# Kernel optimization log

Measured on AMD Instinct MI355X. Metric: run time of the kernel, lower is better.

The kernel has to match this reference:

```python
import jax, jax.numpy as jnp
import numpy as np

N, E, EMB, EDGE, ITERS = 50000, 400000, 128, 32, 2
EPS = 1e-5


def setup_inputs() -> dict:
    key = jax.random.key(0)
    ks = jax.random.split(key, 8)
    s = 0.05

    def lin(k, i, o):
        return jax.random.normal(k, (i, o), jnp.float32) * s

    def mlp_params(k):
        k1, k2 = jax.random.split(k)
        return dict(W1=lin(k1, 2 * EMB + EDGE, EMB), b1=jnp.zeros((EMB,)),
                    g1=jnp.ones((EMB,)), be1=jnp.zeros((EMB,)),
                    W2=lin(k2, EMB, EMB), b2=jnp.zeros((EMB,)),
                    g2=jnp.ones((EMB,)), be2=jnp.zeros((EMB,)))

    p = mlp_params(ks[3])
    c = mlp_params(ks[4])
    inp = {
        'nodes': jax.random.normal(ks[0], (N, EMB), jnp.float32),
        'edges': jax.random.randint(ks[1], (2, E), 0, N, jnp.int64),
        'edge_attr': jax.random.normal(ks[2], (E, EDGE), jnp.float32),
        'fW': lin(ks[5], EMB, EMB), 'fb': jnp.zeros((EMB,)),
        'fg': jnp.ones((EMB,)), 'fbe': jnp.zeros((EMB,)),
    }
    for name, d in (('p', p), ('c', c)):
        for kk, v in d.items():
            inp[name + kk] = v
    return inp


def _bn(x, g, b):
    # training-mode BatchNorm1d: batch stats over axis 0, biased variance
    m = x.mean(0)
    v = x.var(0)
    return (x - m) * jax.lax.rsqrt(v + EPS) * g + b


def _edge_mlp(h, W1, b1, g1, be1, W2, b2, g2, be2):
    h = jax.nn.relu(_bn(h @ W1 + b1, g1, be1))
    return jax.nn.relu(_bn(h @ W2 + b2, g2, be2))


def _agg(x, idx_i, idx_j, ea, params):
    # message: mlp([x_i, x_j, edge_attr]); aggregate sum at idx_i; degree-normalize
    msg = _edge_mlp(jnp.concatenate([x[idx_i], x[idx_j], ea], axis=1), *params)
    summed = jax.ops.segment_sum(msg, idx_i, num_segments=x.shape[0])
    deg = jax.ops.segment_sum(jnp.ones(idx_i.shape, x.dtype), idx_i,
                              num_segments=x.shape[0])
    deg_inv = jnp.where(deg > 0, 1.0 / deg, 0.0)
    return summed * deg_inv[:, None]


def reference(nodes, edges, edge_attr,
              pW1, pb1, pg1, pbe1, pW2, pb2, pg2, pbe2,
              cW1, cb1, cg1, cbe1, cW2, cb2, cg2, cbe2,
              fW, fb, fg, fbe):
    src, dst = edges[0], edges[1]
    pp = (pW1, pb1, pg1, pbe1, pW2, pb2, pg2, pbe2)
    cp = (cW1, cb1, cg1, cbe1, cW2, cb2, cg2, cbe2)
    for _ in range(ITERS):
        fi = _agg(nodes, dst, src, edge_attr, pp)  # parent: source_to_target
        fo = _agg(nodes, src, dst, edge_attr, cp)  # child: target_to_source
        upd = jax.nn.relu(_bn((nodes + fi + fo) @ fW + fb, fg, fbe))
        nodes = nodes + upd
    return nodes
```

## Files before the change

### kernel.cpp

```cpp
#include <hip/hip_runtime.h>
#include <math.h>

#define NN 50000
#define EE 400000
#define EMBD 128
#define KIN 288
#define NITERS 2
#define EPSV 1e-5f
#define SAE 296
#define SA1 136
#define NT_E 6250
#define G0P 1024
#define G1 1024

typedef __attribute__((ext_vector_type(8))) short bf16x8;
typedef __attribute__((ext_vector_type(4))) float f32x4;

#define MFMA16(a, b, c) __builtin_amdgcn_mfma_f32_16x16x32_bf16(a, b, c, 0, 0, 0)

__device__ __forceinline__ unsigned short f2bf(float x) {
  unsigned int u = __float_as_uint(x);
  u += 0x7fffu + ((u >> 16) & 1u);
  return (unsigned short)(u >> 16);
}

__device__ __forceinline__ int physch(int ch, int row) {
  return (ch < 32) ? ((ch & ~7) | ((ch ^ (row & 7)) & 7)) : ch;
}


__global__ void k_zeroi(int* __restrict__ p, int n) {
  for (int i = blockIdx.x * blockDim.x + threadIdx.x; i < n;
       i += gridDim.x * blockDim.x)
    p[i] = 0;
}

__global__ void k_detect(const long long* __restrict__ e64, int* __restrict__ flag) {
  __shared__ int ok;
  if (threadIdx.x == 0) ok = 1;
  __syncthreads();
  for (int i = threadIdx.x; i < 4096; i += blockDim.x) {
    const long long v = e64[i];
    if (v < 0 || v >= NN) atomicAnd(&ok, 0);
  }
  __syncthreads();
  if (threadIdx.x == 0) *flag = ok;
}

__global__ void k_convert(const void* __restrict__ edges, const int* __restrict__ flag,
                          int* __restrict__ src, int* __restrict__ dst) {
  const int is64 = *flag;
  for (int i = blockIdx.x * blockDim.x + threadIdx.x; i < 2 * EE;
       i += gridDim.x * blockDim.x) {
    const int v = is64 ? (int)((const long long*)edges)[i] : ((const int*)edges)[i];
    if (i < EE) src[i] = v; else dst[i - EE] = v;
  }
}

__global__ void k_count(const int* __restrict__ src, const int* __restrict__ dst,
                        int* __restrict__ degp, int* __restrict__ degc) {
  for (int e = blockIdx.x * blockDim.x + threadIdx.x; e < EE;
       e += gridDim.x * blockDim.x) {
    atomicAdd(&degp[dst[e]], 1);
    atomicAdd(&degc[src[e]], 1);
  }
}

__global__ void k_dinv(const int* __restrict__ dp, const int* __restrict__ dc,
                       float* __restrict__ ip, float* __restrict__ ic) {
  for (int n = blockIdx.x * blockDim.x + threadIdx.x; n < NN;
       n += gridDim.x * blockDim.x) {
    ip[n] = dp[n] ? 1.f / (float)dp[n] : 0.f;
    ic[n] = dc[n] ? 1.f / (float)dc[n] : 0.f;
  }
}

__global__ __launch_bounds__(1024) void k_scan2(
    const int* __restrict__ degp, const int* __restrict__ degc,
    int* __restrict__ offp, int* __restrict__ offc) {
  const int* deg = blockIdx.x ? degc : degp;
  int* off = blockIdx.x ? offc : offp;
  __shared__ int sh[1024];
  const int t = threadIdx.x;
  const int i0 = t * 49;
  int s = 0;
#pragma unroll 1
  for (int k = 0; k < 49; ++k) {
    const int i = i0 + k;
    if (i < NN) s += deg[i];
  }
  sh[t] = s;
  __syncthreads();
  for (int o = 1; o < 1024; o <<= 1) {
    const int y = (t >= o) ? sh[t - o] : 0;
    __syncthreads();
    sh[t] += y;
    __syncthreads();
  }
  int base = sh[t] - s;
#pragma unroll 1
  for (int k = 0; k < 49; ++k) {
    const int i = i0 + k;
    if (i < NN) {
      off[i] = base;
      base += deg[i];
    }
  }
  if (t == 1023) off[NN] = sh[1023];
}

__global__ void k_copycur(const int* __restrict__ offp, const int* __restrict__ offc,
                          int* __restrict__ curp, int* __restrict__ curc) {
  for (int i = blockIdx.x * blockDim.x + threadIdx.x; i < NN;
       i += gridDim.x * blockDim.x) {
    curp[i] = offp[i];
    curc[i] = offc[i];
  }
}

__global__ void k_scatter(const int* __restrict__ src, const int* __restrict__ dst,
                          int* __restrict__ curp, int* __restrict__ curc,
                          int* __restrict__ lstp, int* __restrict__ lstc) {
  for (int e = blockIdx.x * blockDim.x + threadIdx.x; e < EE;
       e += gridDim.x * blockDim.x) {
    const int pp = atomicAdd(&curp[dst[e]], 1);
    lstp[pp] = e;
    const int pc = atomicAdd(&curc[src[e]], 1);
    lstc[pc] = e;
  }
}

__global__ void k_initnodes(const float* __restrict__ in, float* __restrict__ nd,
                            unsigned short* __restrict__ xb) {
  const int tot = NN * EMBD / 4;
  for (int i = blockIdx.x * blockDim.x + threadIdx.x; i < tot;
       i += gridDim.x * blockDim.x) {
    const float4 v = ((const float4*)in)[i];
    ((float4*)nd)[i] = v;
    short4 b;
    b.x = (short)f2bf(v.x); b.y = (short)f2bf(v.y);
    b.z = (short)f2bf(v.z); b.w = (short)f2bf(v.w);
    *(short4*)&xb[(size_t)i * 4] = b;
  }
}

__global__ void k_prepW(const float* __restrict__ W, unsigned short* __restrict__ Wt,
                        int K) {
  const int idx = blockIdx.x * blockDim.x + threadIdx.x;
  if (idx < K * EMBD) {
    const int k = idx >> 7, n = idx & 127;
    Wt[(size_t)n * K + k] = f2bf(W[(size_t)k * EMBD + n]);
  }
}

__global__ void k_prepea(const float* __restrict__ ea,
                         unsigned short* __restrict__ eab) {
  const int tot = EE * 32 / 8;
  for (int i = blockIdx.x * blockDim.x + threadIdx.x; i < tot;
       i += gridDim.x * blockDim.x) {
    const float4 a = ((const float4*)ea)[i * 2];
    const float4 b = ((const float4*)ea)[i * 2 + 1];
    union { unsigned short u[8]; uint4 v; } o;
    o.u[0] = f2bf(a.x); o.u[1] = f2bf(a.y); o.u[2] = f2bf(a.z); o.u[3] = f2bf(a.w);
    o.u[4] = f2bf(b.x); o.u[5] = f2bf(b.y); o.u[6] = f2bf(b.z); o.u[7] = f2bf(b.w);
    ((uint4*)eab)[i] = o.v;
  }
}


template <int EAB>
__global__ __launch_bounds__(256, 1) void k_pass0m(
    const unsigned short* __restrict__ xb,
    const int* __restrict__ i0, const int* __restrict__ j0,
    const unsigned short* __restrict__ W0, float* __restrict__ st0,
    unsigned short* __restrict__ Y0,
    const int* __restrict__ i1, const int* __restrict__ j1,
    const unsigned short* __restrict__ W1, float* __restrict__ st1,
    unsigned short* __restrict__ Y1,
    const float* __restrict__ ea, const unsigned short* __restrict__ eab,
    const int nb0) {
  __shared__ __align__(16) unsigned short Ab[64 * SAE];
  __shared__ float red[256];
  const int phase = (blockIdx.x >= nb0) ? 1 : 0;
  const int* __restrict__ idx_i = phase ? i1 : i0;
  const int* __restrict__ idx_j = phase ? j1 : j0;
  const unsigned short* __restrict__ W1t = phase ? W1 : W0;
  float* __restrict__ stat = phase ? st1 : st0;
  unsigned short* __restrict__ Y = phase ? Y1 : Y0;
  const int stride = phase ? ((int)gridDim.x - nb0) : nb0;
  const int t = threadIdx.x;
  const int lane = t & 63, w = t >> 6, m = lane & 15, kg = lane >> 4;
  const int r = t >> 2, sub = t & 3;
  const int n0 = w * 32 + m, n1 = n0 + 16;
  bf16x8 B0[9], B1[9];
#pragma unroll
  for (int ks = 0; ks < 9; ++ks) {
    B0[ks] = *(const bf16x8*)&W1t[(size_t)n0 * KIN + ks * 32 + kg * 8];
    B1[ks] = *(const bf16x8*)&W1t[(size_t)n1 * KIN + ks * 32 + kg * 8];
  }
  float s0 = 0.f, s1 = 0.f, q0 = 0.f, q1 = 0.f;
  int tile = blockIdx.x - phase * nb0;
  int inext = idx_i[tile * 64 + r];
  int jnext = idx_j[tile * 64 + r];
  while (tile < NT_E) {
    const int icur = inext, jcur = jnext;
    __syncthreads();
    {
      const uint4* xi = (const uint4*)(xb + (size_t)icur * EMBD);
      const uint4* xj = (const uint4*)(xb + (size_t)jcur * EMBD);
      unsigned short* rowp = &Ab[r * SAE];
#pragma unroll
      for (int qq = 0; qq < 8; ++qq) {
        const int c = sub + qq * 4;
        const uint4 v = (c < 16) ? xi[c] : xj[c - 16];
        *(uint4*)&rowp[physch(c, r) * 8] = v;
      }
      const int e = tile * 64 + r;
      uint4 ev;
      if (EAB) {
        ev = *(const uint4*)&eab[(size_t)e * 32 + sub * 8];
      } else {
        const float4 e0 = *(const float4*)&ea[(size_t)e * 32 + sub * 8];
        const float4 e1 = *(const float4*)&ea[(size_t)e * 32 + sub * 8 + 4];
        union { unsigned short u[8]; uint4 v4; } o;
        o.u[0] = f2bf(e0.x); o.u[1] = f2bf(e0.y); o.u[2] = f2bf(e0.z);
        o.u[3] = f2bf(e0.w); o.u[4] = f2bf(e1.x); o.u[5] = f2bf(e1.y);
        o.u[6] = f2bf(e1.z); o.u[7] = f2bf(e1.w);
        ev = o.v4;
      }
      *(uint4*)&rowp[(32 + sub) * 8] = ev;
    }
    __syncthreads();
    const int next = tile + stride;
    if (next < NT_E) {
      inext = idx_i[next * 64 + r];
      jnext = idx_j[next * 64 + r];
    }
    const f32x4 zz = {0.f, 0.f, 0.f, 0.f};
    f32x4 acc[4][2] = {{zz, zz}, {zz, zz}, {zz, zz}, {zz, zz}};
#pragma unroll
    for (int ks = 0; ks < 9; ++ks) {
      const int aoff = physch(ks * 4 + kg, m) * 8;
#pragma unroll
      for (int mt = 0; mt < 4; ++mt) {
        const bf16x8 a = *(const bf16x8*)&Ab[(mt * 16 + m) * SAE + aoff];
        acc[mt][0] = MFMA16(a, B0[ks], acc[mt][0]);
        acc[mt][1] = MFMA16(a, B1[ks], acc[mt][1]);
      }
    }
#pragma unroll
    for (int mt = 0; mt < 4; ++mt)
#pragma unroll
      for (int r2 = 0; r2 < 4; ++r2) {
        const float v0 = acc[mt][0][r2], v1 = acc[mt][1][r2];
        s0 += v0; q0 += v0 * v0;
        s1 += v1; q1 += v1 * v1;
      }
    __syncthreads();
#pragma unroll
    for (int nt = 0; nt < 2; ++nt) {
      const int c = w * 32 + nt * 16 + m;
      const int cc = c >> 3, cl = c & 7;
#pragma unroll
      for (int mt = 0; mt < 4; ++mt)
#pragma unroll
        for (int r2 = 0; r2 < 4; ++r2) {
          const int rw = mt * 16 + kg * 4 + r2;
          Ab[rw * SAE + physch(cc, rw) * 8 + cl] = f2bf(acc[mt][nt][r2]);
        }
    }
    __syncthreads();
    unsigned short* Yt = Y + (size_t)tile * 64 * EMBD;
#pragma unroll
    for (int i = 0; i < 4; ++i) {
      const int g = i * 2048 + t * 8;
      const int row = g >> 7, ch = (g >> 3) & 15;
      *(uint4*)&Yt[g] = *(const uint4*)&Ab[row * SAE + physch(ch, row) * 8];
    }
    tile = next;
  }
  s0 += __shfl_xor(s0, 16); s0 += __shfl_xor(s0, 32);
  q0 += __shfl_xor(q0, 16); q0 += __shfl_xor(q0, 32);
  s1 += __shfl_xor(s1, 16); s1 += __shfl_xor(s1, 32);
  q1 += __shfl_xor(q1, 16); q1 += __shfl_xor(q1, 32);
  if (kg == 0) {
    const int c0 = w * 32 + m, c1 = c0 + 16;
    red[c0] = s0; red[128 + c0] = q0;
    red[c1] = s1; red[128 + c1] = q1;
  }
  __syncthreads();
  if (t < 128) {
    atomicAdd(&stat[t], red[t]);
    atomicAdd(&stat[128 + t], red[128 + t]);
  }
}


__device__ __forceinline__ void pass1_body(
    const unsigned short* __restrict__ W2t, float* __restrict__ stat,
    unsigned short* __restrict__ Y, int tile, const int stride) {
  __shared__ __align__(16) unsigned short Ab[64 * SA1];
  __shared__ float red[256];
  const int t = threadIdx.x;
  const int lane = t & 63, w = t >> 6, m = lane & 15, kg = lane >> 4;
  const int n0 = w * 32 + m, n1 = n0 + 16;
  const int ch = t & 15;
  bf16x8 B0[4], B1[4];
#pragma unroll
  for (int ks = 0; ks < 4; ++ks) {
    B0[ks] = *(const bf16x8*)&W2t[(size_t)n0 * EMBD + ks * 32 + kg * 8];
    B1[ks] = *(const bf16x8*)&W2t[(size_t)n1 * EMBD + ks * 32 + kg * 8];
  }
  float scr[8], shr[8];
#pragma unroll
  for (int h = 0; h < 8; ++h) {
    scr[h] = stat[256 + ch * 8 + h];
    shr[h] = stat[384 + ch * 8 + h];
  }
  float s0 = 0.f, s1 = 0.f, q0 = 0.f, q1 = 0.f;
  uint4 yreg[4];
  {
    const unsigned short* Yt = Y + (size_t)tile * 64 * EMBD;
#pragma unroll
    for (int i = 0; i < 4; ++i)
      yreg[i] = *(const uint4*)&Yt[i * 2048 + t * 8];
  }
  while (tile < NT_E) {
    __syncthreads();
#pragma unroll
    for (int i = 0; i < 4; ++i) {
      const int row = i * 16 + (t >> 4);
      const unsigned int* pv = (const unsigned int*)&yreg[i];
      union { unsigned short u[8]; uint4 v; } o;
#pragma unroll
      for (int h = 0; h < 4; ++h) {
        const unsigned int pw = pv[h];
        const float f0 = __uint_as_float(pw << 16);
        const float f1 = __uint_as_float(pw & 0xffff0000u);
        o.u[h * 2] = f2bf(fmaxf(fmaf(f0, scr[h * 2], shr[h * 2]), 0.f));
        o.u[h * 2 + 1] = f2bf(fmaxf(fmaf(f1, scr[h * 2 + 1], shr[h * 2 + 1]), 0.f));
      }
      *(uint4*)&Ab[row * SA1 + physch(ch, row) * 8] = o.v;
    }
    __syncthreads();
    const int next = tile + stride;
    if (next < NT_E) {
      const unsigned short* Yt = Y + (size_t)next * 64 * EMBD;
#pragma unroll
      for (int i = 0; i < 4; ++i)
        yreg[i] = *(const uint4*)&Yt[i * 2048 + t * 8];
    }
    const f32x4 zz = {0.f, 0.f, 0.f, 0.f};
    f32x4 acc[4][2] = {{zz, zz}, {zz, zz}, {zz, zz}, {zz, zz}};
#pragma unroll
    for (int ks = 0; ks < 4; ++ks) {
      const int aoff = physch(ks * 4 + kg, m) * 8;
#pragma unroll
      for (int mt = 0; mt < 4; ++mt) {
        const bf16x8 a = *(const bf16x8*)&Ab[(mt * 16 + m) * SA1 + aoff];
        acc[mt][0] = MFMA16(a, B0[ks], acc[mt][0]);
        acc[mt][1] = MFMA16(a, B1[ks], acc[mt][1]);
      }
    }
#pragma unroll
    for (int mt = 0; mt < 4; ++mt)
#pragma unroll
      for (int r2 = 0; r2 < 4; ++r2) {
        const float v0 = acc[mt][0][r2], v1 = acc[mt][1][r2];
        s0 += v0; q0 += v0 * v0;
        s1 += v1; q1 += v1 * v1;
      }
    __syncthreads();
#pragma unroll
    for (int nt = 0; nt < 2; ++nt) {
      const int c = w * 32 + nt * 16 + m;
      const int cc = c >> 3, cl = c & 7;
#pragma unroll
      for (int mt = 0; mt < 4; ++mt)
#pragma unroll
        for (int r2 = 0; r2 < 4; ++r2) {
          const int rw = mt * 16 + kg * 4 + r2;
          Ab[rw * SA1 + physch(cc, rw) * 8 + cl] = f2bf(acc[mt][nt][r2]);
        }
    }
    __syncthreads();
    unsigned short* Yo = Y + (size_t)tile * 64 * EMBD;
#pragma unroll
    for (int i = 0; i < 4; ++i) {
      const int g = i * 2048 + t * 8;
      const int row = g >> 7, c2 = (g >> 3) & 15;
      *(uint4*)&Yo[g] = *(const uint4*)&Ab[row * SA1 + physch(c2, row) * 8];
    }
    tile = next;
  }
  s0 += __shfl_xor(s0, 16); s0 += __shfl_xor(s0, 32);
  q0 += __shfl_xor(q0, 16); q0 += __shfl_xor(q0, 32);
  s1 += __shfl_xor(s1, 16); s1 += __shfl_xor(s1, 32);
  q1 += __shfl_xor(q1, 16); q1 += __shfl_xor(q1, 32);
  if (kg == 0) {
    const int c0 = w * 32 + m, c1 = c0 + 16;
    red[c0] = s0; red[128 + c0] = q0;
    red[c1] = s1; red[128 + c1] = q1;
  }
  __syncthreads();
  if (t < 128) {
    atomicAdd(&stat[512 + t], red[t]);
    atomicAdd(&stat[640 + t], red[128 + t]);
  }
}

__global__ __launch_bounds__(256, 3) void k_pass1(
    const unsigned short* __restrict__ W2t, float* __restrict__ stat,
    unsigned short* __restrict__ Y) {
  pass1_body(W2t, stat, Y, blockIdx.x, G1);
}

__global__ __launch_bounds__(256, 3) void k_pass1m(
    const unsigned short* __restrict__ Wp, const unsigned short* __restrict__ Wc,
    float* __restrict__ statP, float* __restrict__ statC,
    unsigned short* __restrict__ Yp, unsigned short* __restrict__ Yc) {
  const int phase = (blockIdx.x >= G1) ? 1 : 0;
  const unsigned short* W2t = phase ? Wc : Wp;
  float* stat = phase ? statC : statP;
  unsigned short* Y = phase ? Yc : Yp;
  pass1_body(W2t, stat, Y, blockIdx.x - phase * G1, G1);
}


__global__ __launch_bounds__(256) void k_aggm(
    const unsigned short* __restrict__ Yp, const unsigned short* __restrict__ Yc,
    const int* __restrict__ offp, const int* __restrict__ lstp,
    const int* __restrict__ offc, const int* __restrict__ lstc,
    const float* __restrict__ statP, const float* __restrict__ statC,
    const float* __restrict__ dinvp, const float* __restrict__ dinvc,
    float* __restrict__ agg) {
  const int n = blockIdx.x * 4 + (threadIdx.x >> 6);
  const int lane = threadIdx.x & 63;
  if (n >= NN) return;
  float r0, r1;
  {
    const int o0 = offp[n], o1 = offp[n + 1];
    const float sc0 = statP[768 + 2 * lane], sc1 = statP[768 + 2 * lane + 1];
    const float sh0 = statP[896 + 2 * lane], sh1 = statP[896 + 2 * lane + 1];
    float a0 = 0.f, a1 = 0.f;
    for (int o = o0; o < o1; ++o) {
      const int e = lstp[o];
      const unsigned int pw = ((const unsigned int*)(Yp + (size_t)e * EMBD))[lane];
      a0 += fmaxf(fmaf(__uint_as_float(pw << 16), sc0, sh0), 0.f);
      a1 += fmaxf(fmaf(__uint_as_float(pw & 0xffff0000u), sc1, sh1), 0.f);
    }
    const float d = dinvp[n];
    r0 = a0 * d;
    r1 = a1 * d;
  }
  {
    const int o0 = offc[n], o1 = offc[n + 1];
    const float sc0 = statC[768 + 2 * lane], sc1 = statC[768 + 2 * lane + 1];
    const float sh0 = statC[896 + 2 * lane], sh1 = statC[896 + 2 * lane + 1];
    float a0 = 0.f, a1 = 0.f;
    for (int o = o0; o < o1; ++o) {
      const int e = lstc[o];
      const unsigned int pw = ((const unsigned int*)(Yc + (size_t)e * EMBD))[lane];
      a0 += fmaxf(fmaf(__uint_as_float(pw << 16), sc0, sh0), 0.f);
      a1 += fmaxf(fmaf(__uint_as_float(pw & 0xffff0000u), sc1, sh1), 0.f);
    }
    const float d = dinvc[n];
    r0 += a0 * d;
    r1 += a1 * d;
  }
  float2 out;
  out.x = r0;
  out.y = r1;
  ((float2*)(agg + (size_t)n * EMBD))[lane] = out;
}

template <int ADD>
__global__ __launch_bounds__(256) void k_agg2(
    const unsigned short* __restrict__ Y2, const int* __restrict__ off,
    const int* __restrict__ lst, const float* __restrict__ stat,
    const float* __restrict__ dinv, float* __restrict__ agg) {
  const int n = blockIdx.x * 4 + (threadIdx.x >> 6);
  const int lane = threadIdx.x & 63;
  if (n >= NN) return;
  const int o0 = off[n], o1 = off[n + 1];
  const float sc0 = stat[768 + 2 * lane], sc1 = stat[768 + 2 * lane + 1];
  const float sh0 = stat[896 + 2 * lane], sh1 = stat[896 + 2 * lane + 1];
  float a0 = 0.f, a1 = 0.f;
  for (int o = o0; o < o1; ++o) {
    const int e = lst[o];
    const unsigned int pw = ((const unsigned int*)(Y2 + (size_t)e * EMBD))[lane];
    a0 += fmaxf(fmaf(__uint_as_float(pw << 16), sc0, sh0), 0.f);
    a1 += fmaxf(fmaf(__uint_as_float(pw & 0xffff0000u), sc1, sh1), 0.f);
  }
  const float d = dinv[n];
  float2 out;
  if (ADD) {
    const float2 prev = ((const float2*)(agg + (size_t)n * EMBD))[lane];
    out.x = prev.x + a0 * d;
    out.y = prev.y + a1 * d;
  } else {
    out.x = a0 * d;
    out.y = a1 * d;
  }
  ((float2*)(agg + (size_t)n * EMBD))[lane] = out;
}


template <int NK, bool SWZ>
__device__ __forceinline__ void gemm_g(const unsigned short* Ab, const int sa,
                                       const unsigned short* __restrict__ Wt,
                                       const int K, const int m, const int kg,
                                       const int w, f32x4 acc[4][2]) {
  const int n0 = w * 32 + m, n1 = n0 + 16;
#pragma unroll
  for (int ks = 0; ks < NK; ++ks) {
    const int koff = ks * 32 + kg * 8;
    const int aoff = SWZ ? physch(koff >> 3, m) * 8 : koff;
    const bf16x8 b0 = *(const bf16x8*)&Wt[(size_t)n0 * K + koff];
    const bf16x8 b1 = *(const bf16x8*)&Wt[(size_t)n1 * K + koff];
#pragma unroll
    for (int mt = 0; mt < 4; ++mt) {
      const bf16x8 a = *(const bf16x8*)&Ab[(mt * 16 + m) * sa + aoff];
      acc[mt][0] = MFMA16(a, b0, acc[mt][0]);
      acc[mt][1] = MFMA16(a, b1, acc[mt][1]);
    }
  }
}

__device__ __forceinline__ void stats_epi64(const f32x4 acc[4][2], float* red,
                                            float* __restrict__ statg, const int t,
                                            const int m, const int kg, const int w) {
#pragma unroll
  for (int nt = 0; nt < 2; ++nt) {
    float s = 0.f, q = 0.f;
#pragma unroll
    for (int mt = 0; mt < 4; ++mt)
#pragma unroll
      for (int r = 0; r < 4; ++r) {
        const float v = acc[mt][nt][r];
        s += v;
        q += v * v;
      }
    s += __shfl_xor(s, 16); s += __shfl_xor(s, 32);
    q += __shfl_xor(q, 16); q += __shfl_xor(q, 32);
    if (kg == 0) {
      const int c = w * 32 + nt * 16 + m;
      red[c] = s;
      red[128 + c] = q;
    }
  }
  __syncthreads();
  if (t < 128) {
    atomicAdd(&statg[t], red[t]);
    atomicAdd(&statg[128 + t], red[128 + t]);
  }
}

__global__ __launch_bounds__(256) void k_node(
    const float* __restrict__ nd, float* __restrict__ ag,
    const unsigned short* __restrict__ Wt, float* __restrict__ stat) {
  __shared__ __align__(16) unsigned short Ab[64 * SA1];
  __shared__ float red[256];
  const int t = threadIdx.x;
  const int n0 = blockIdx.x * 64;
  {
    const int r = t >> 2, sub = t & 3;
    const int row = n0 + r;
    unsigned short* drow = &Ab[r * SA1];
#pragma unroll
    for (int q = 0; q < 8; ++q) {
      const int c4 = sub + q * 4;
      float4 va;
      if (row < NN) {
        va = ((const float4*)(nd + (size_t)row * EMBD))[c4];
        const float4 vb = ((const float4*)(ag + (size_t)row * EMBD))[c4];
        va.x += vb.x; va.y += vb.y; va.z += vb.z; va.w += vb.w;
      } else {
        va.x = va.y = va.z = va.w = 0.f;
      }
      short4 b;
      b.x = (short)f2bf(va.x); b.y = (short)f2bf(va.y);
      b.z = (short)f2bf(va.z); b.w = (short)f2bf(va.w);
      *(short4*)&drow[c4 * 4] = b;
    }
  }
  __syncthreads();
  const int lane = t & 63, w = t >> 6, m = lane & 15, kg = lane >> 4;
  const f32x4 zz = {0.f, 0.f, 0.f, 0.f};
  f32x4 acc[4][2] = {{zz, zz}, {zz, zz}, {zz, zz}, {zz, zz}};
  gemm_g<4, false>(Ab, SA1, Wt, EMBD, m, kg, w, acc);
#pragma unroll
  for (int nt = 0; nt < 2; ++nt) {
    const int c = w * 32 + nt * 16 + m;
#pragma unroll
    for (int mt = 0; mt < 4; ++mt)
#pragma unroll
      for (int r = 0; r < 4; ++r) {
        const int row = n0 + mt * 16 + kg * 4 + r;
        if (row < NN) ag[(size_t)row * EMBD + c] = acc[mt][nt][r];
      }
  }
  stats_epi64(acc, red, stat, t, m, kg, w);
}


__device__ __forceinline__ void finalize_one(float* __restrict__ sb,
                                             const float* __restrict__ g,
                                             const float* __restrict__ be,
                                             float cnt, int c) {
  const float s = sb[c], sq = sb[EMBD + c];
  const float m = s / cnt;
  float v = sq / cnt - m * m;
  v = fmaxf(v, 0.f);
  const float rs = rsqrtf(v + EPSV);
  const float sc = g[c] * rs;
  sb[256 + c] = sc;
  sb[384 + c] = be[c] - m * sc;
  sb[c] = 0.f;
  sb[EMBD + c] = 0.f;
}

__global__ void k_finalize(float* __restrict__ statbase, const float* __restrict__ g,
                           const float* __restrict__ be, float cnt) {
  const int t = threadIdx.x;
  if (t < EMBD) finalize_one(statbase, g, be, cnt, t);
}

__global__ void k_finalize2(float* __restrict__ sA, const float* __restrict__ gA,
                            const float* __restrict__ bA, float* __restrict__ sB,
                            const float* __restrict__ gB, const float* __restrict__ bB,
                            float cnt) {
  const int t = threadIdx.x;
  if (t < EMBD) finalize_one(sA, gA, bA, cnt, t);
  else finalize_one(sB, gB, bB, cnt, t - EMBD);
}

__global__ void k_update(float* __restrict__ nd, unsigned short* __restrict__ xb,
                         const float* __restrict__ Z, const float* __restrict__ stat) {
  const float* sc = stat + 256;
  const float* sh = stat + 384;
  const int total = NN * EMBD / 4;
  for (int i = blockIdx.x * blockDim.x + threadIdx.x; i < total;
       i += gridDim.x * blockDim.x) {
    const int c4 = i & 31;
    const float4 v = ((const float4*)Z)[i];
    const float4 s4 = ((const float4*)sc)[c4];
    const float4 h4 = ((const float4*)sh)[c4];
    float4 nv = ((float4*)nd)[i];
    nv.x += fmaxf(fmaf(v.x, s4.x, h4.x), 0.f);
    nv.y += fmaxf(fmaf(v.y, s4.y, h4.y), 0.f);
    nv.z += fmaxf(fmaf(v.z, s4.z, h4.z), 0.f);
    nv.w += fmaxf(fmaf(v.w, s4.w, h4.w), 0.f);
    ((float4*)nd)[i] = nv;
    short4 b;
    b.x = (short)f2bf(nv.x); b.y = (short)f2bf(nv.y);
    b.z = (short)f2bf(nv.z); b.w = (short)f2bf(nv.w);
    *(short4*)&xb[(size_t)i * 4] = b;
  }
}


extern "C" void kernel_launch(void* const* d_in, const int* in_sizes, int n_in,
                              void* d_out, int out_size, void* d_ws, size_t ws_size,
                              hipStream_t stream) {
  const float* in_nodes = (const float*)d_in[0];
  const void* edges = d_in[1];
  const float* ea = (const float*)d_in[2];
  const float* fW = (const float*)d_in[3];
  const float* fg = (const float*)d_in[5];
  const float* fbe = (const float*)d_in[6];
  const float* p_[8];
  const float* c_[8];
  for (int i = 0; i < 8; ++i) {
    p_[i] = (const float*)d_in[7 + i];
    c_[i] = (const float*)d_in[15 + i];
  }
  float* nodes = (float*)d_out;

  char* base = (char*)d_ws;
  size_t cur = 0;
  auto take = [&](size_t bytes) -> void* {
    void* p = base + cur;
    cur = (cur + bytes + 255) & ~(size_t)255;
    return p;
  };
  float* agg = (float*)take((size_t)NN * EMBD * 4);
  unsigned short* xb = (unsigned short*)take((size_t)NN * EMBD * 2);
  int* src = (int*)take(EE * 4);
  int* dst = (int*)take(EE * 4);
  int* lstp = (int*)take(EE * 4);
  int* lstc = (int*)take(EE * 4);
  int* offp = (int*)take((NN + 1) * 4);
  int* offc = (int*)take((NN + 1) * 4);
  int* curp = (int*)take(NN * 4);
  int* curc = (int*)take(NN * 4);
  float* dinvp = (float*)take(NN * 4);
  float* dinvc = (float*)take(NN * 4);
  float* stat = (float*)take(2048 * 4);
  int* flag = (int*)take(4);
  unsigned short* pW1t = (unsigned short*)take((size_t)EMBD * KIN * 2);
  unsigned short* pW2t = (unsigned short*)take((size_t)EMBD * EMBD * 2);
  unsigned short* cW1t = (unsigned short*)take((size_t)EMBD * KIN * 2);
  unsigned short* cW2t = (unsigned short*)take((size_t)EMBD * EMBD * 2);
  unsigned short* fWt = (unsigned short*)take((size_t)EMBD * EMBD * 2);
  unsigned short* Y1p = (unsigned short*)take((size_t)EE * EMBD * 2);
  const size_t y_bytes = (size_t)EE * EMBD * 2;
  const bool useM = (cur + y_bytes) <= ws_size;
  unsigned short* Y1c = useM ? (unsigned short*)take(y_bytes) : nullptr;
  const size_t eab_bytes = (size_t)EE * 32 * 2;
  const bool useEab = (cur + eab_bytes) <= ws_size;
  unsigned short* eab = useEab ? (unsigned short*)take(eab_bytes) : nullptr;

  k_zeroi<<<64, 256, 0, stream>>>((int*)stat, 2048);
  k_zeroi<<<128, 256, 0, stream>>>(curp, NN);
  k_zeroi<<<128, 256, 0, stream>>>(curc, NN);
  k_detect<<<1, 256, 0, stream>>>((const long long*)edges, flag);
  k_convert<<<1024, 256, 0, stream>>>(edges, flag, src, dst);
  k_count<<<1024, 256, 0, stream>>>(src, dst, curp, curc);
  k_dinv<<<128, 256, 0, stream>>>(curp, curc, dinvp, dinvc);
  k_scan2<<<2, 1024, 0, stream>>>(curp, curc, offp, offc);
  k_copycur<<<128, 256, 0, stream>>>(offp, offc, curp, curc);
  k_scatter<<<1024, 256, 0, stream>>>(src, dst, curp, curc, lstp, lstc);
  k_initnodes<<<2048, 256, 0, stream>>>(in_nodes, nodes, xb);
  k_prepW<<<(KIN * EMBD + 255) / 256, 256, 0, stream>>>(p_[0], pW1t, KIN);
  k_prepW<<<(EMBD * EMBD + 255) / 256, 256, 0, stream>>>(p_[4], pW2t, EMBD);
  k_prepW<<<(KIN * EMBD + 255) / 256, 256, 0, stream>>>(c_[0], cW1t, KIN);
  k_prepW<<<(EMBD * EMBD + 255) / 256, 256, 0, stream>>>(c_[4], cW2t, EMBD);
  k_prepW<<<(EMBD * EMBD + 255) / 256, 256, 0, stream>>>(fW, fWt, EMBD);
  if (useEab) k_prepea<<<2048, 256, 0, stream>>>(ea, eab);

  const int NB = (NN + 63) / 64;
  float* statP = stat;
  float* statC = stat + 1024;

  for (int it = 0; it < NITERS; ++it) {
    if (useM) {
      if (useEab)
        k_pass0m<1><<<2 * G0P, 256, 0, stream>>>(
            xb, dst, src, pW1t, statP, Y1p, src, dst, cW1t, statC, Y1c,
            ea, eab, G0P);
      else
        k_pass0m<0><<<2 * G0P, 256, 0, stream>>>(
            xb, dst, src, pW1t, statP, Y1p, src, dst, cW1t, statC, Y1c,
            ea, eab, G0P);
      k_finalize2<<<1, 256, 0, stream>>>(statP, p_[2], p_[3],
                                         statC, c_[2], c_[3], (float)EE);
      k_pass1m<<<2 * G1, 256, 0, stream>>>(pW2t, cW2t, statP, statC, Y1p, Y1c);
      k_finalize2<<<1, 256, 0, stream>>>(statP + 512, p_[6], p_[7],
                                         statC + 512, c_[6], c_[7], (float)EE);
      k_aggm<<<NN / 4, 256, 0, stream>>>(Y1p, Y1c, offp, lstp, offc, lstc,
                                         statP, statC, dinvp, dinvc, agg);
    } else {
      if (useEab)
        k_pass0m<1><<<G0P, 256, 0, stream>>>(
            xb, dst, src, pW1t, statP, Y1p, dst, src, pW1t, statP, Y1p,
            ea, eab, G0P);
      else
        k_pass0m<0><<<G0P, 256, 0, stream>>>(
            xb, dst, src, pW1t, statP, Y1p, dst, src, pW1t, statP, Y1p,
            ea, eab, G0P);
      k_finalize<<<1, 128, 0, stream>>>(statP, p_[2], p_[3], (float)EE);
      k_pass1<<<G1, 256, 0, stream>>>(pW2t, statP, Y1p);
      k_finalize<<<1, 128, 0, stream>>>(statP + 512, p_[6], p_[7], (float)EE);
      k_agg2<0><<<NN / 4, 256, 0, stream>>>(Y1p, offp, lstp, statP, dinvp, agg);
      if (useEab)
        k_pass0m<1><<<G0P, 256, 0, stream>>>(
            xb, src, dst, cW1t, statP, Y1p, src, dst, cW1t, statP, Y1p,
            ea, eab, G0P);
      else
        k_pass0m<0><<<G0P, 256, 0, stream>>>(
            xb, src, dst, cW1t, statP, Y1p, src, dst, cW1t, statP, Y1p,
            ea, eab, G0P);
      k_finalize<<<1, 128, 0, stream>>>(statP, c_[2], c_[3], (float)EE);
      k_pass1<<<G1, 256, 0, stream>>>(cW2t, statP, Y1p);
      k_finalize<<<1, 128, 0, stream>>>(statP + 512, c_[6], c_[7], (float)EE);
      k_agg2<1><<<NN / 4, 256, 0, stream>>>(Y1p, offc, lstc, statP, dinvc, agg);
    }
    k_node<<<NB, 256, 0, stream>>>(nodes, agg, fWt, statP);
    k_finalize<<<1, 128, 0, stream>>>(statP, fg, fbe, (float)NN);
    k_update<<<2048, 256, 0, stream>>>(nodes, xb, agg, statP);
  }
}
```

Baseline: 986.5 us.

## Prefetch next tile's gathered rows into registers and use nontemporal Y traffic

The first edge-MLP kernel now gathers the next tile's x_i/x_j rows and edge attributes into registers right after the shared-memory fill, so the gather latency overlaps the MFMA work instead of stalling before each tile. Stores and loads of the intermediate Y buffers in the GEMM and aggregation kernels are switched to nontemporal variants to reduce cache pollution by streaming data. The prefetch adds about 36 VGPRs per thread, which may reduce occupancy. Nontemporal hints could also hurt if Y would otherwise have been reused from L2/MALL.

Measured after the change: 1.219 ms. 1.24x slower.

```diff
diff --git a/kernel.cpp b/kernel.cpp
--- a/kernel.cpp
+++ b/kernel.cpp
@@ -15,6 +15,7 @@
 
 typedef __attribute__((ext_vector_type(8))) short bf16x8;
 typedef __attribute__((ext_vector_type(4))) float f32x4;
+typedef __attribute__((ext_vector_type(4))) unsigned int u32x4;
 
 #define MFMA16(a, b, c) __builtin_amdgcn_mfma_f32_16x16x32_bf16(a, b, c, 0, 0, 0)
 
@@ -26,6 +27,13 @@
 
 __device__ __forceinline__ int physch(int ch, int row) {
   return (ch < 32) ? ((ch & ~7) | ((ch ^ (row & 7)) & 7)) : ch;
+}
+
+__device__ __forceinline__ u32x4 ntld4(const void* p) {
+  return __builtin_nontemporal_load((const u32x4*)p);
+}
+__device__ __forceinline__ void ntst4(void* p, u32x4 v) {
+  __builtin_nontemporal_store(v, (u32x4*)p);
 }
 
 
@@ -200,25 +208,55 @@
   }
   float s0 = 0.f, s1 = 0.f, q0 = 0.f, q1 = 0.f;
   int tile = blockIdx.x - phase * nb0;
-  int inext = idx_i[tile * 64 + r];
-  int jnext = idx_j[tile * 64 + r];
+  uint4 xreg[8];
+  uint4 earg;
+  {
+    const int e = tile * 64 + r;
+    const int i = idx_i[e], j = idx_j[e];
+    const uint4* xi = (const uint4*)(xb + (size_t)i * EMBD);
+    const uint4* xj = (const uint4*)(xb + (size_t)j * EMBD);
+#pragma unroll
+    for (int qq = 0; qq < 8; ++qq) {
+      const int c = sub + qq * 4;
+      xreg[qq] = (c < 16) ? xi[c] : xj[c - 16];
+    }
+    if (EAB) {
+      earg = *(const uint4*)&eab[(size_t)e * 32 + sub * 8];
+    } else {
+      const float4 e0 = *(const float4*)&ea[(size_t)e * 32 + sub * 8];
+      const float4 e1 = *(const float4*)&ea[(size_t)e * 32 + sub * 8 + 4];
+      union { unsigned short u[8]; uint4 v4; } o;
+      o.u[0] = f2bf(e0.x); o.u[1] = f2bf(e0.y); o.u[2] = f2bf(e0.z);
+      o.u[3] = f2bf(e0.w); o.u[4] = f2bf(e1.x); o.u[5] = f2bf(e1.y);
+      o.u[6] = f2bf(e1.z); o.u[7] = f2bf(e1.w);
+      earg = o.v4;
+    }
+  }
   while (tile < NT_E) {
-    const int icur = inext, jcur = jnext;
     __syncthreads();
     {
-      const uint4* xi = (const uint4*)(xb + (size_t)icur * EMBD);
-      const uint4* xj = (const uint4*)(xb + (size_t)jcur * EMBD);
       unsigned short* rowp = &Ab[r * SAE];
 #pragma unroll
       for (int qq = 0; qq < 8; ++qq) {
         const int c = sub + qq * 4;
-        const uint4 v = (c < 16) ? xi[c] : xj[c - 16];
-        *(uint4*)&rowp[physch(c, r) * 8] = v;
-      }
-      const int e = tile * 64 + r;
-      uint4 ev;
+        *(uint4*)&rowp[physch(c, r) * 8] = xreg[qq];
+      }
+      *(uint4*)&rowp[(32 + sub) * 8] = earg;
+    }
+    __syncthreads();
+    const int next = tile + stride;
+    if (next < NT_E) {
+      const int e = next * 64 + r;
+      const int i = idx_i[e], j = idx_j[e];
+      const uint4* xi = (const uint4*)(xb + (size_t)i * EMBD);
+      const uint4* xj = (const uint4*)(xb + (size_t)j * EMBD);
+#pragma unroll
+      for (int qq = 0; qq < 8; ++qq) {
+        const int c = sub + qq * 4;
+        xreg[qq] = (c < 16) ? xi[c] : xj[c - 16];
+      }
       if (EAB) {
-        ev = *(const uint4*)&eab[(size_t)e * 32 + sub * 8];
+        earg = *(const uint4*)&eab[(size_t)e * 32 + sub * 8];
       } else {
         const float4 e0 = *(const float4*)&ea[(size_t)e * 32 + sub * 8];
         const float4 e1 = *(const float4*)&ea[(size_t)e * 32 + sub * 8 + 4];
@@ -226,15 +264,8 @@
         o.u[0] = f2bf(e0.x); o.u[1] = f2bf(e0.y); o.u[2] = f2bf(e0.z);
         o.u[3] = f2bf(e0.w); o.u[4] = f2bf(e1.x); o.u[5] = f2bf(e1.y);
         o.u[6] = f2bf(e1.z); o.u[7] = f2bf(e1.w);
-        ev = o.v4;
-      }
-      *(uint4*)&rowp[(32 + sub) * 8] = ev;
-    }
-    __syncthreads();
-    const int next = tile + stride;
-    if (next < NT_E) {
-      inext = idx_i[next * 64 + r];
-      jnext = idx_j[next * 64 + r];
+        earg = o.v4;
+      }
     }
     const f32x4 zz = {0.f, 0.f, 0.f, 0.f};
     f32x4 acc[4][2] = {{zz, zz}, {zz, zz}, {zz, zz}, {zz, zz}};
@@ -275,7 +306,7 @@
     for (int i = 0; i < 4; ++i) {
       const int g = i * 2048 + t * 8;
       const int row = g >> 7, ch = (g >> 3) & 15;
-      *(uint4*)&Yt[g] = *(const uint4*)&Ab[row * SAE + physch(ch, row) * 8];
+      ntst4(&Yt[g], *(const u32x4*)&Ab[row * SAE + physch(ch, row) * 8]);
     }
     tile = next;
   }
@@ -318,23 +349,22 @@
     shr[h] = stat[384 + ch * 8 + h];
   }
   float s0 = 0.f, s1 = 0.f, q0 = 0.f, q1 = 0.f;
-  uint4 yreg[4];
+  u32x4 yreg[4];
   {
     const unsigned short* Yt = Y + (size_t)tile * 64 * EMBD;
 #pragma unroll
     for (int i = 0; i < 4; ++i)
-      yreg[i] = *(const uint4*)&Yt[i * 2048 + t * 8];
+      yreg[i] = ntld4(&Yt[i * 2048 + t * 8]);
   }
   while (tile < NT_E) {
     __syncthreads();
 #pragma unroll
     for (int i = 0; i < 4; ++i) {
       const int row = i * 16 + (t >> 4);
-      const unsigned int* pv = (const unsigned int*)&yreg[i];
       union { unsigned short u[8]; uint4 v; } o;
 #pragma unroll
       for (int h = 0; h < 4; ++h) {
-        const unsigned int pw = pv[h];
+        const unsigned int pw = yreg[i][h];
         const float f0 = __uint_as_float(pw << 16);
         const float f1 = __uint_as_float(pw & 0xffff0000u);
         o.u[h * 2] = f2bf(fmaxf(fmaf(f0, scr[h * 2], shr[h * 2]), 0.f));
@@ -348,7 +378,7 @@
       const unsigned short* Yt = Y + (size_t)next * 64 * EMBD;
 #pragma unroll
       for (int i = 0; i < 4; ++i)
-        yreg[i] = *(const uint4*)&Yt[i * 2048 + t * 8];
+        yreg[i] = ntld4(&Yt[i * 2048 + t * 8]);
     }
     const f32x4 zz = {0.f, 0.f, 0.f, 0.f};
     f32x4 acc[4][2] = {{zz, zz}, {zz, zz}, {zz, zz}, {zz, zz}};
@@ -389,7 +419,7 @@
     for (int i = 0; i < 4; ++i) {
       const int g = i * 2048 + t * 8;
       const int row = g >> 7, c2 = (g >> 3) & 15;
-      *(uint4*)&Yo[g] = *(const uint4*)&Ab[row * SA1 + physch(c2, row) * 8];
+      ntst4(&Yo[g], *(const u32x4*)&Ab[row * SA1 + physch(c2, row) * 8]);
     }
     tile = next;
   }
@@ -445,7 +475,8 @@
     float a0 = 0.f, a1 = 0.f;
     for (int o = o0; o < o1; ++o) {
       const int e = lstp[o];
-      const unsigned int pw = ((const unsigned int*)(Yp + (size_t)e * EMBD))[lane];
+      const unsigned int pw = __builtin_nontemporal_load(
+          &((const unsigned int*)(Yp + (size_t)e * EMBD))[lane]);
       a0 += fmaxf(fmaf(__uint_as_float(pw << 16), sc0, sh0), 0.f);
       a1 += fmaxf(fmaf(__uint_as_float(pw & 0xffff0000u), sc1, sh1), 0.f);
     }
@@ -460,7 +491,8 @@
     float a0 = 0.f, a1 = 0.f;
     for (int o = o0; o < o1; ++o) {
       const int e = lstc[o];
-      const unsigned int pw = ((const unsigned int*)(Yc + (size_t)e * EMBD))[lane];
+      const unsigned int pw = __builtin_nontemporal_load(
+          &((const unsigned int*)(Yc + (size_t)e * EMBD))[lane]);
       a0 += fmaxf(fmaf(__uint_as_float(pw << 16), sc0, sh0), 0.f);
       a1 += fmaxf(fmaf(__uint_as_float(pw & 0xffff0000u), sc1, sh1), 0.f);
     }
@@ -488,7 +520,8 @@
   float a0 = 0.f, a1 = 0.f;
   for (int o = o0; o < o1; ++o) {
     const int e = lst[o];
-    const unsigned int pw = ((const unsigned int*)(Y2 + (size_t)e * EMBD))[lane];
+    const unsigned int pw = __builtin_nontemporal_load(
+        &((const unsigned int*)(Y2 + (size_t)e * EMBD))[lane]);
     a0 += fmaxf(fmaf(__uint_as_float(pw << 16), sc0, sh0), 0.f);
     a1 += fmaxf(fmaf(__uint_as_float(pw & 0xffff0000u), sc1, sh1), 0.f);
   }
```

## Process edges in CSR-sorted order so aggregation reads contiguous message rows

Applied to the files above, without the earlier changes.

The edge-MLP first pass now visits edges through the CSR permutation list, so the message buffer Y is written in segment-sorted order. The aggregation kernels can then read rows contiguously by CSR offset instead of gathering them through the edge list. This trades one extra indirection plus a scattered edge-attribute read in the GEMM pass for sequential, coalesced reads in the aggregation. Because rows sharing a destination now sit together, the xi gathers may also get better cache reuse.

Result: faster. 935.9 us (-5.1%).

```diff
diff --git a/kernel.cpp b/kernel.cpp
--- a/kernel.cpp
+++ b/kernel.cpp
@@ -171,17 +171,18 @@
 template <int EAB>
 __global__ __launch_bounds__(256, 1) void k_pass0m(
     const unsigned short* __restrict__ xb,
-    const int* __restrict__ i0, const int* __restrict__ j0,
-    const unsigned short* __restrict__ W0, float* __restrict__ st0,
-    unsigned short* __restrict__ Y0,
-    const int* __restrict__ i1, const int* __restrict__ j1,
-    const unsigned short* __restrict__ W1, float* __restrict__ st1,
-    unsigned short* __restrict__ Y1,
+    const int* __restrict__ l0, const int* __restrict__ i0,
+    const int* __restrict__ j0, const unsigned short* __restrict__ W0,
+    float* __restrict__ st0, unsigned short* __restrict__ Y0,
+    const int* __restrict__ l1, const int* __restrict__ i1,
+    const int* __restrict__ j1, const unsigned short* __restrict__ W1,
+    float* __restrict__ st1, unsigned short* __restrict__ Y1,
     const float* __restrict__ ea, const unsigned short* __restrict__ eab,
     const int nb0) {
   __shared__ __align__(16) unsigned short Ab[64 * SAE];
   __shared__ float red[256];
   const int phase = (blockIdx.x >= nb0) ? 1 : 0;
+  const int* __restrict__ lst = phase ? l1 : l0;
   const int* __restrict__ idx_i = phase ? i1 : i0;
   const int* __restrict__ idx_j = phase ? j1 : j0;
   const unsigned short* __restrict__ W1t = phase ? W1 : W0;
@@ -200,10 +201,11 @@
   }
   float s0 = 0.f, s1 = 0.f, q0 = 0.f, q1 = 0.f;
   int tile = blockIdx.x - phase * nb0;
-  int inext = idx_i[tile * 64 + r];
-  int jnext = idx_j[tile * 64 + r];
+  int enext = lst[tile * 64 + r];
+  int inext = idx_i[enext];
+  int jnext = idx_j[enext];
   while (tile < NT_E) {
-    const int icur = inext, jcur = jnext;
+    const int ecur = enext, icur = inext, jcur = jnext;
     __syncthreads();
     {
       const uint4* xi = (const uint4*)(xb + (size_t)icur * EMBD);
@@ -215,13 +217,12 @@
         const uint4 v = (c < 16) ? xi[c] : xj[c - 16];
         *(uint4*)&rowp[physch(c, r) * 8] = v;
       }
-      const int e = tile * 64 + r;
       uint4 ev;
       if (EAB) {
-        ev = *(const uint4*)&eab[(size_t)e * 32 + sub * 8];
+        ev = *(const uint4*)&eab[(size_t)ecur * 32 + sub * 8];
       } else {
-        const float4 e0 = *(const float4*)&ea[(size_t)e * 32 + sub * 8];
-        const float4 e1 = *(const float4*)&ea[(size_t)e * 32 + sub * 8 + 4];
+        const float4 e0 = *(const float4*)&ea[(size_t)ecur * 32 + sub * 8];
+        const float4 e1 = *(const float4*)&ea[(size_t)ecur * 32 + sub * 8 + 4];
         union { unsigned short u[8]; uint4 v4; } o;
         o.u[0] = f2bf(e0.x); o.u[1] = f2bf(e0.y); o.u[2] = f2bf(e0.z);
         o.u[3] = f2bf(e0.w); o.u[4] = f2bf(e1.x); o.u[5] = f2bf(e1.y);
@@ -233,8 +234,9 @@
     __syncthreads();
     const int next = tile + stride;
     if (next < NT_E) {
-      inext = idx_i[next * 64 + r];
-      jnext = idx_j[next * 64 + r];
+      enext = lst[next * 64 + r];
+      inext = idx_i[enext];
+      jnext = idx_j[enext];
     }
     const f32x4 zz = {0.f, 0.f, 0.f, 0.f};
     f32x4 acc[4][2] = {{zz, zz}, {zz, zz}, {zz, zz}, {zz, zz}};
@@ -429,8 +431,7 @@
 
 __global__ __launch_bounds__(256) void k_aggm(
     const unsigned short* __restrict__ Yp, const unsigned short* __restrict__ Yc,
-    const int* __restrict__ offp, const int* __restrict__ lstp,
-    const int* __restrict__ offc, const int* __restrict__ lstc,
+    const int* __restrict__ offp, const int* __restrict__ offc,
     const float* __restrict__ statP, const float* __restrict__ statC,
     const float* __restrict__ dinvp, const float* __restrict__ dinvc,
     float* __restrict__ agg) {
@@ -444,8 +445,7 @@
     const float sh0 = statP[896 + 2 * lane], sh1 = statP[896 + 2 * lane + 1];
     float a0 = 0.f, a1 = 0.f;
     for (int o = o0; o < o1; ++o) {
-      const int e = lstp[o];
-      const unsigned int pw = ((const unsigned int*)(Yp + (size_t)e * EMBD))[lane];
+      const unsigned int pw = ((const unsigned int*)(Yp + (size_t)o * EMBD))[lane];
       a0 += fmaxf(fmaf(__uint_as_float(pw << 16), sc0, sh0), 0.f);
       a1 += fmaxf(fmaf(__uint_as_float(pw & 0xffff0000u), sc1, sh1), 0.f);
     }
@@ -459,8 +459,7 @@
     const float sh0 = statC[896 + 2 * lane], sh1 = statC[896 + 2 * lane + 1];
     float a0 = 0.f, a1 = 0.f;
     for (int o = o0; o < o1; ++o) {
-      const int e = lstc[o];
-      const unsigned int pw = ((const unsigned int*)(Yc + (size_t)e * EMBD))[lane];
+      const unsigned int pw = ((const unsigned int*)(Yc + (size_t)o * EMBD))[lane];
       a0 += fmaxf(fmaf(__uint_as_float(pw << 16), sc0, sh0), 0.f);
       a1 += fmaxf(fmaf(__uint_as_float(pw & 0xffff0000u), sc1, sh1), 0.f);
     }
@@ -477,8 +476,8 @@
 template <int ADD>
 __global__ __launch_bounds__(256) void k_agg2(
     const unsigned short* __restrict__ Y2, const int* __restrict__ off,
-    const int* __restrict__ lst, const float* __restrict__ stat,
-    const float* __restrict__ dinv, float* __restrict__ agg) {
+    const float* __restrict__ stat, const float* __restrict__ dinv,
+    float* __restrict__ agg) {
   const int n = blockIdx.x * 4 + (threadIdx.x >> 6);
   const int lane = threadIdx.x & 63;
   if (n >= NN) return;
@@ -487,8 +486,7 @@
   const float sh0 = stat[896 + 2 * lane], sh1 = stat[896 + 2 * lane + 1];
   float a0 = 0.f, a1 = 0.f;
   for (int o = o0; o < o1; ++o) {
-    const int e = lst[o];
-    const unsigned int pw = ((const unsigned int*)(Y2 + (size_t)e * EMBD))[lane];
+    const unsigned int pw = ((const unsigned int*)(Y2 + (size_t)o * EMBD))[lane];
     a0 += fmaxf(fmaf(__uint_as_float(pw << 16), sc0, sh0), 0.f);
     a1 += fmaxf(fmaf(__uint_as_float(pw & 0xffff0000u), sc1, sh1), 0.f);
   }
@@ -737,44 +735,44 @@
     if (useM) {
       if (useEab)
         k_pass0m<1><<<2 * G0P, 256, 0, stream>>>(
-            xb, dst, src, pW1t, statP, Y1p, src, dst, cW1t, statC, Y1c,
-            ea, eab, G0P);
+            xb, lstp, dst, src, pW1t, statP, Y1p,
+            lstc, src, dst, cW1t, statC, Y1c, ea, eab, G0P);
       else
         k_pass0m<0><<<2 * G0P, 256, 0, stream>>>(
-            xb, dst, src, pW1t, statP, Y1p, src, dst, cW1t, statC, Y1c,
-            ea, eab, G0P);
+            xb, lstp, dst, src, pW1t, statP, Y1p,
+            lstc, src, dst, cW1t, statC, Y1c, ea, eab, G0P);
       k_finalize2<<<1, 256, 0, stream>>>(statP, p_[2], p_[3],
                                          statC, c_[2], c_[3], (float)EE);
       k_pass1m<<<2 * G1, 256, 0, stream>>>(pW2t, cW2t, statP, statC, Y1p, Y1c);
       k_finalize2<<<1, 256, 0, stream>>>(statP + 512, p_[6], p_[7],
                                          statC + 512, c_[6], c_[7], (float)EE);
-      k_aggm<<<NN / 4, 256, 0, stream>>>(Y1p, Y1c, offp, lstp, offc, lstc,
+      k_aggm<<<NN / 4, 256, 0, stream>>>(Y1p, Y1c, offp, offc,
                                          statP, statC, dinvp, dinvc, agg);
     } else {
       if (useEab)
         k_pass0m<1><<<G0P, 256, 0, stream>>>(
-            xb, dst, src, pW1t, statP, Y1p, dst, src, pW1t, statP, Y1p,
-            ea, eab, G0P);
+            xb, lstp, dst, src, pW1t, statP, Y1p,
+            lstp, dst, src, pW1t, statP, Y1p, ea, eab, G0P);
       else
         k_pass0m<0><<<G0P, 256, 0, stream>>>(
-            xb, dst, src, pW1t, statP, Y1p, dst, src, pW1t, statP, Y1p,
-            ea, eab, G0P);
+            xb, lstp, dst, src, pW1t, statP, Y1p,
+            lstp, dst, src, pW1t, statP, Y1p, ea, eab, G0P);
       k_finalize<<<1, 128, 0, stream>>>(statP, p_[2], p_[3], (float)EE);
       k_pass1<<<G1, 256, 0, stream>>>(pW2t, statP, Y1p);
       k_finalize<<<1, 128, 0, stream>>>(statP + 512, p_[6], p_[7], (float)EE);
-      k_agg2<0><<<NN / 4, 256, 0, stream>>>(Y1p, offp, lstp, statP, dinvp, agg);
+      k_agg2<0><<<NN / 4, 256, 0, stream>>>(Y1p, offp, statP, dinvp, agg);
       if (useEab)
         k_pass0m<1><<<G0P, 256, 0, stream>>>(
-            xb, src, dst, cW1t, statP, Y1p, src, dst, cW1t, statP, Y1p,
-            ea, eab, G0P);
+            xb, lstc, src, dst, cW1t, statP, Y1p,
+            lstc, src, dst, cW1t, statP, Y1p, ea, eab, G0P);
       else
         k_pass0m<0><<<G0P, 256, 0, stream>>>(
-            xb, src, dst, cW1t, statP, Y1p, src, dst, cW1t, statP, Y1p,
-            ea, eab, G0P);
+            xb, lstc, src, dst, cW1t, statP, Y1p,
+            lstc, src, dst, cW1t, statP, Y1p, ea, eab, G0P);
       k_finalize<<<1, 128, 0, stream>>>(statP, c_[2], c_[3], (float)EE);
       k_pass1<<<G1, 256, 0, stream>>>(cW2t, statP, Y1p);
       k_finalize<<<1, 128, 0, stream>>>(statP + 512, c_[6], c_[7], (float)EE);
-      k_agg2<1><<<NN / 4, 256, 0, stream>>>(Y1p, offc, lstc, statP, dinvc, agg);
+      k_agg2<1><<<NN / 4, 256, 0, stream>>>(Y1p, offc, statP, dinvc, agg);
     }
     k_node<<<NB, 256, 0, stream>>>(nodes, agg, fWt, statP);
     k_finalize<<<1, 128, 0, stream>>>(statP, fg, fbe, (float)NN);
```
